# Optimization experiments

Hardware: AMD Instinct MI355X
Metric: run time of the kernel (lower is better)

The kernel has to match this reference:

```python
import jax, jax.numpy as jnp
import numpy as np
from jax import lax

DG, KH, KW = 8, 3, 3
STRIDE, PAD, DIL = 1, 1, 1


def setup_inputs() -> dict:
    key = jax.random.key(0)
    ks = jax.random.split(key, 6)
    B, C, H, W = 4, 256, 64, 64
    Cout = 256
    off_ch = DG * 3 * KH * KW  # 216
    x = jax.random.normal(ks[0], (B, C, H, W), dtype=jnp.float32)
    extra_feat = jax.random.normal(ks[1], (B, C, H, W), dtype=jnp.float32)
    weight = jax.random.normal(ks[2], (Cout, C, KH, KW), dtype=jnp.float32) * 0.02
    bias = jax.random.normal(ks[3], (Cout,), dtype=jnp.float32) * 0.01
    off_w = jax.random.normal(ks[4], (off_ch, C, KH, KW), dtype=jnp.float32) * 0.01
    off_b = jax.random.normal(ks[5], (off_ch,), dtype=jnp.float32) * 0.01
    return {"x": x, "extra_feat": extra_feat, "weight": weight, "bias": bias,
            "off_w": off_w, "off_b": off_b}


def _modulated_deform_conv(x, offset, mask, weight, bias):
    B, C, H, W = x.shape
    Cout = weight.shape[0]
    K = KH * KW
    Ho, Wo = offset.shape[2], offset.shape[3]
    Cg = C // DG

    # offset: [B, 2*DG*K, Ho, Wo] interpreted as (dg, K, (dy, dx)) interleaved
    off = offset.reshape(B, DG, K, 2, Ho, Wo)
    dy, dx = off[:, :, :, 0], off[:, :, :, 1]  # [B, DG, K, Ho, Wo]

    ky = jnp.repeat(jnp.arange(KH), KW)  # [K]
    kx = jnp.tile(jnp.arange(KW), KH)    # [K]
    base_y = (jnp.arange(Ho) * STRIDE - PAD)[None, None, None, :, None] + (ky * DIL)[None, None, :, None, None]
    base_x = (jnp.arange(Wo) * STRIDE - PAD)[None, None, None, None, :] + (kx * DIL)[None, None, :, None, None]
    py = dy + base_y  # [B, DG, K, Ho, Wo]
    px = dx + base_x

    y0f = jnp.floor(py)
    x0f = jnp.floor(px)
    fy = py - y0f
    fx = px - x0f
    y0 = y0f.astype(jnp.int32)
    x0 = x0f.astype(jnp.int32)

    xg = x.reshape(B, DG, Cg, H * W)
    N = K * Ho * Wo

    def gather(yi, xi):
        valid = ((yi >= 0) & (yi < H) & (xi >= 0) & (xi < W)).astype(x.dtype)
        idx = (jnp.clip(yi, 0, H - 1) * W + jnp.clip(xi, 0, W - 1)).reshape(B, DG, 1, N)
        g = jnp.take_along_axis(xg, jnp.broadcast_to(idx, (B, DG, Cg, N)), axis=-1)
        g = g.reshape(B, DG, Cg, K, Ho, Wo)
        return g * valid[:, :, None]

    val = (((1 - fy) * (1 - fx))[:, :, None] * gather(y0, x0)
           + ((1 - fy) * fx)[:, :, None] * gather(y0, x0 + 1)
           + (fy * (1 - fx))[:, :, None] * gather(y0 + 1, x0)
           + (fy * fx)[:, :, None] * gather(y0 + 1, x0 + 1))
    val = val * mask.reshape(B, DG, 1, K, Ho, Wo)
    val = val.reshape(B, C, K, Ho, Wo)

    out = jnp.einsum('bckhw,ock->bohw', val, weight.reshape(Cout, C, K))
    return out + bias[None, :, None, None]


def reference(x, extra_feat, weight, bias, off_w, off_b):
    # conv_offset: plain conv predicting offsets + mask
    om = lax.conv_general_dilated(
        extra_feat, off_w, window_strides=(STRIDE, STRIDE),
        padding=((PAD, PAD), (PAD, PAD)), rhs_dilation=(DIL, DIL),
        dimension_numbers=('NCHW', 'OIHW', 'NCHW')) + off_b[None, :, None, None]
    o1, o2, mask = jnp.split(om, 3, axis=1)
    offset = jnp.concatenate([o1, o2], axis=1)
    mask = jax.nn.sigmoid(mask)
    return _modulated_deform_conv(x, offset, mask, weight, bias)
```

## Files before the change

### kernel.cpp

```cpp
#include <hip/hip_runtime.h>
#include <hip/hip_bf16.h>
#include <math.h>

#define BB 4
#define CC 256
#define HH 64
#define WW 64
#define HW 4096
#define PH 68
#define PW 68
#define COUT 256
#define OFFC 216
#define KTOT 2304
#define NCHUNK 72

typedef __attribute__((ext_vector_type(4))) float f32x4;
typedef __attribute__((ext_vector_type(8))) short s16x8;
typedef __attribute__((ext_vector_type(8))) unsigned short u16x8;
typedef __attribute__((ext_vector_type(2))) unsigned int u32x2;

__device__ __forceinline__ unsigned short f2bf(float f) {
    unsigned int u = __float_as_uint(f);
    return (unsigned short)((u + 0x7fffu + ((u >> 16) & 1u)) >> 16);
}
__device__ __forceinline__ float bflo(unsigned int u) { return __uint_as_float(u << 16); }
__device__ __forceinline__ float bfhi(unsigned int u) { return __uint_as_float(u & 0xffff0000u); }
__device__ __forceinline__ unsigned int pkbf(float a, float b) {
    __hip_bfloat162 h = __float22bfloat162_rn(make_float2(a, b));
    unsigned int r;
    __builtin_memcpy(&r, &h, 4);
    return r;
}

#define WAITL() asm volatile("s_waitcnt lgkmcnt(0)" ::: "memory")
#define RBAR() __builtin_amdgcn_s_barrier()

__global__ __launch_bounds__(256) void pack_w_main(const float* __restrict__ w,
                                                   unsigned short* __restrict__ wp) {
    int idx = blockIdx.x * 256 + threadIdx.x;
    int t = idx >> 13, r = idx & 8191;
    int oc = r >> 5, s = (r >> 3) & 3, e = r & 7;
    int kk = ((s ^ ((oc >> 1) & 3)) << 3) | e;
    int dg = t / 9, tap = t - dg * 9;
    int c = dg * 32 + kk;
    wp[idx] = f2bf(w[((size_t)oc * CC + c) * 9 + tap]);
}

__global__ __launch_bounds__(256) void pack_w_off(const float* __restrict__ w,
                                                  unsigned short* __restrict__ wp) {
    int idx = blockIdx.x * 256 + threadIdx.x;
    int t = idx >> 13, r = idx & 8191;
    int oc = r >> 5, s = (r >> 3) & 3, e = r & 7;
    int kk = ((s ^ ((oc >> 1) & 3)) << 3) | e;
    int tap = t >> 3, cg = t & 7;
    int c = cg * 32 + kk;
    float v = (oc < OFFC) ? w[((size_t)oc * CC + c) * 9 + tap] : 0.f;
    wp[idx] = f2bf(v);
}

__global__ __launch_bounds__(256) void pad_tr2(const float* __restrict__ srcx,
                                               const float* __restrict__ srce,
                                               unsigned short* __restrict__ dx_,
                                               unsigned short* __restrict__ de_) {
    const float* src = blockIdx.y ? srce : srcx;
    unsigned short* dst = blockIdx.y ? de_ : dx_;
    int blk = blockIdx.x;
    int b = blk / PH, yp = blk % PH;
    int y = yp - 2;
    unsigned short* drow = dst + ((size_t)b * PH + yp) * PW * CC;
    int tid = threadIdx.x;
    if ((unsigned)y >= (unsigned)HH) {
        for (int i = tid; i < PW * CC / 8; i += 256) *(u16x8*)&drow[(size_t)i * 8] = (u16x8)0;
        return;
    }
    __shared__ float tile[64][65];
    int lane = tid & 63, w = tid >> 6;
    int oct = tid & 7, xi = tid >> 3;
    const float* srow = src + (size_t)b * CC * HW + (size_t)y * WW;
    for (int chunk = 0; chunk < 4; chunk++) {
        __syncthreads();
#pragma unroll
        for (int i = 0; i < 16; i++) {
            int c = chunk * 64 + w * 16 + i;
            tile[w * 16 + i][lane] = srow[(size_t)c * HW + lane];
        }
        __syncthreads();
#pragma unroll
        for (int xq = 0; xq < 3; xq++) {
            int xp = xq * 32 + xi;
            if (xp < PW) {
                int x = xp - 2;
                u16x8 v = (u16x8)0;
                if ((unsigned)x < (unsigned)WW) {
#pragma unroll
                    for (int e = 0; e < 8; e++) v[e] = f2bf(tile[oct * 8 + e][x]);
                }
                *(u16x8*)&drow[(size_t)xp * CC + chunk * 64 + oct * 8] = v;
            }
        }
    }
}


#define A_LOAD(WPP, T, AF)                                                \
    {                                                                     \
        const unsigned short* wt_ = WPP + (size_t)(T) * 8192 + aoff;      \
        AF[0] = *(const s16x8*)&wt_[0];                                   \
        AF[1] = *(const s16x8*)&wt_[512];                                 \
        AF[2] = *(const s16x8*)&wt_[8192];                                \
        AF[3] = *(const s16x8*)&wt_[8704];                                \
    }

#define MFMA8R(AC, BUF)                                                                      \
    {                                                                                        \
        int sw_ = (lg ^ ((r16 >> 1) & 3)) << 3;                                              \
        s16x8 b0_ = *(const s16x8*)&sB[BUF][0][r16 * 32 + sw_];                              \
        s16x8 b1_ = *(const s16x8*)&sB[BUF][0][(16 + r16) * 32 + sw_];                       \
        acc[0][0] = __builtin_amdgcn_mfma_f32_16x16x32_bf16(AC[0], b0_, acc[0][0], 0, 0, 0); \
        acc[0][1] = __builtin_amdgcn_mfma_f32_16x16x32_bf16(AC[0], b1_, acc[0][1], 0, 0, 0); \
        acc[1][0] = __builtin_amdgcn_mfma_f32_16x16x32_bf16(AC[1], b0_, acc[1][0], 0, 0, 0); \
        acc[1][1] = __builtin_amdgcn_mfma_f32_16x16x32_bf16(AC[1], b1_, acc[1][1], 0, 0, 0); \
        b0_ = *(const s16x8*)&sB[BUF][1][r16 * 32 + sw_];                                    \
        b1_ = *(const s16x8*)&sB[BUF][1][(16 + r16) * 32 + sw_];                             \
        acc[0][0] = __builtin_amdgcn_mfma_f32_16x16x32_bf16(AC[2], b0_, acc[0][0], 0, 0, 0); \
        acc[0][1] = __builtin_amdgcn_mfma_f32_16x16x32_bf16(AC[2], b1_, acc[0][1], 0, 0, 0); \
        acc[1][0] = __builtin_amdgcn_mfma_f32_16x16x32_bf16(AC[3], b0_, acc[1][0], 0, 0, 0); \
        acc[1][1] = __builtin_amdgcn_mfma_f32_16x16x32_bf16(AC[3], b1_, acc[1][1], 0, 0, 0); \
    }

__global__ __launch_bounds__(512, 4) void fused_dcn(const unsigned short* __restrict__ eT,
                                                    const unsigned short* __restrict__ xT,
                                                    const unsigned short* __restrict__ wpo,
                                                    const unsigned short* __restrict__ wpm,
                                                    const float* __restrict__ off_b,
                                                    const float* __restrict__ bias,
                                                    float* __restrict__ out) {
    __shared__ __align__(16) unsigned short sB[2][2][1024];
    __shared__ unsigned int sOP[NCHUNK][32][3];

    int bx = blockIdx.x;
    int b = bx >> 6, y = bx & 63;
    int pxh = blockIdx.y;
    int tid = threadIdx.x;
    int lane = tid & 63;
    int w = tid >> 6;
    int r16 = lane & 15, lg = lane >> 4;
    int aoff = (w * 32 + r16) * 32 + ((lg ^ ((r16 >> 1) & 3)) << 3);
    int p1px = tid >> 4, ch2 = tid & 15;
    int pxg = pxh * 32 + p1px;
    int kt = tid >> 8;
    int p2px = (tid >> 3) & 31;
    int ch4 = tid & 7;

    const unsigned short* eb = eT + (size_t)b * PH * PW * CC;
    const unsigned short* xb = xT + (size_t)b * PH * PW * CC;

    f32x4 acc[2][2];
#pragma unroll
    for (int mi = 0; mi < 2; mi++)
#pragma unroll
        for (int ni = 0; ni < 2; ni++) acc[mi][ni] = (f32x4)0.f;

    s16x8 aA[4], aB[4];

#define BSLOT2 (p1px * 32 + ((((ch2 >> 2) ^ ((p1px >> 1) & 3))) << 3) + (ch2 & 3) * 2)
#define OF_B(T, BV)                                                                          \
    {                                                                                        \
        int tap_ = (T) >> 3, cg_ = (T) & 7;                                                  \
        int ky_ = tap_ / 3, kx_ = tap_ - ky_ * 3;                                            \
        BV = *(const unsigned int*)&eb[(size_t)((y + ky_ + 1) * PW + (pxg + kx_ + 1)) * CC + \
                                       cg_ * 32 + ch2 * 2];                                  \
    }
#define OF_ITF(T, BUF, AC, AN, BP0, BP1, BN0, BN1)               \
    {                                                            \
        A_LOAD(wpo, (T) + 2, AN)                                 \
        OF_B((T) + 4, BN0)                                       \
        OF_B((T) + 5, BN1)                                       \
        MFMA8R(AC, BUF)                                          \
        *(unsigned int*)&sB[(BUF) ^ 1][0][BSLOT2] = BP0;         \
        *(unsigned int*)&sB[(BUF) ^ 1][1][BSLOT2] = BP1;         \
        WAITL();                                                 \
        RBAR();                                                  \
    }

    {
        unsigned int bP0, bP1, bN0, bN1;
        {
            A_LOAD(wpo, 0, aA)
            unsigned int c0, c1;
            OF_B(0, c0)
            OF_B(1, c1)
            *(unsigned int*)&sB[0][0][BSLOT2] = c0;
            *(unsigned int*)&sB[0][1][BSLOT2] = c1;
            OF_B(2, bP0)
            OF_B(3, bP1)
            WAITL();
            RBAR();
        }
        for (int t = 0; t < 68; t += 4) {
            OF_ITF(t, 0, aA, aB, bP0, bP1, bN0, bN1)
            OF_ITF(t + 2, 1, aB, aA, bN0, bN1, bP0, bP1)
        }
        {
            A_LOAD(wpo, 70, aB)
            MFMA8R(aA, 0)
            *(unsigned int*)&sB[1][0][BSLOT2] = bP0;
            *(unsigned int*)&sB[1][1][BSLOT2] = bP1;
            WAITL();
            RBAR();
        }
        MFMA8R(aB, 1)
    }

    __syncthreads();
#pragma unroll
    for (int mi = 0; mi < 2; mi++) {
#pragma unroll
        for (int ni = 0; ni < 2; ni++) {
#pragma unroll
            for (int j = 0; j < 4; j++) {
                int oc = w * 32 + mi * 16 + lg * 4 + j;
                if (oc < OFFC) {
                    int dg, tap, comp;
                    if (oc < 144) {
                        dg = oc / 18;
                        int rr = oc - dg * 18;
                        tap = rr >> 1;
                        comp = rr & 1;
                    } else {
                        int o2 = oc - 144;
                        dg = o2 / 9;
                        tap = o2 - dg * 9;
                        comp = 2;
                    }
                    sOP[dg * 9 + tap][ni * 16 + r16][comp] =
                        __float_as_uint(acc[mi][ni][j] + off_b[oc]);
                }
            }
        }
    }
    __syncthreads();
    for (int i = tid; i < NCHUNK * 32; i += 512) {
        int tt = i >> 5, px = i & 31;
        int dg = (tt * 57) >> 9;
        int tap = tt - dg * 9;
        int ky = tap / 3, kx = tap - ky * 3;
        float dyv = __uint_as_float(sOP[tt][px][0]);
        float dxv = __uint_as_float(sOP[tt][px][1]);
        float mr = __uint_as_float(sOP[tt][px][2]);
        int xg = pxh * 32 + px;
        float mv = 1.f / (1.f + __expf(-mr));
        float py = (float)(y + ky - 1) + dyv;
        float pxx = (float)(xg + kx - 1) + dxv;
        float y0f = floorf(py), x0f = floorf(pxx);
        float fy = py - y0f, fx = pxx - x0f;
        int yp0 = min(max((int)y0f + 2, 0), PH - 1);
        int yp1 = min(max((int)y0f + 3, 0), PH - 1);
        int xp0 = min(max((int)x0f + 2, 0), PW - 1);
        int xp1 = min(max((int)x0f + 3, 0), PW - 1);
        float w00 = (1.f - fy) * (1.f - fx) * mv;
        float w01 = (1.f - fy) * fx * mv;
        float w10 = fy * (1.f - fx) * mv;
        float w11 = fy * fx * mv;
        sOP[tt][px][0] = (unsigned int)(yp0 * PW + xp0) | ((unsigned int)(xp1 - xp0) << 13) |
                         ((unsigned int)(yp1 - yp0) << 14);
        sOP[tt][px][1] = pkbf(w00, w01);
        sOP[tt][px][2] = pkbf(w10, w11);
    }
    __syncthreads();

#pragma unroll
    for (int mi = 0; mi < 2; mi++)
#pragma unroll
        for (int ni = 0; ni < 2; ni++) acc[mi][ni] = (f32x4)0.f;

#define BSLOT4 (p2px * 32 + ((((ch4 >> 1) ^ ((p2px >> 1) & 3))) << 3) + (ch4 & 1) * 4)
#define DC_G(T, G00, G01, G10, G11)                                       \
    {                                                                     \
        int dg_ = ((T) * 57) >> 9;                                        \
        unsigned int iv_ = sOP[T][p2px][0];                               \
        int o00_ = (int)(iv_ & 8191u) << 8;                               \
        int dxe_ = (int)((iv_ >> 13) & 1u) << 8;                          \
        int dye_ = ((iv_ >> 14) & 1u) ? (PW * CC) : 0;                    \
        const unsigned short* p_ = xb + dg_ * 32 + ch4 * 4;               \
        G00 = *(const u32x2*)(p_ + o00_);                                 \
        G01 = *(const u32x2*)(p_ + o00_ + dxe_);                          \
        G10 = *(const u32x2*)(p_ + o00_ + dye_);                          \
        G11 = *(const u32x2*)(p_ + o00_ + dye_ + dxe_);                   \
    }
#define DC_FIN(T, G00, G01, G10, G11, BUF)                                                \
    {                                                                                     \
        unsigned int wa_ = sOP[T][p2px][1];                                               \
        unsigned int wb_ = sOP[T][p2px][2];                                               \
        float w00 = bflo(wa_), w01 = bfhi(wa_);                                           \
        float w10 = bflo(wb_), w11 = bfhi(wb_);                                           \
        float v0 = w00 * bflo(G00[0]) + w01 * bflo(G01[0]) + w10 * bflo(G10[0]) +         \
                   w11 * bflo(G11[0]);                                                    \
        float v1 = w00 * bfhi(G00[0]) + w01 * bfhi(G01[0]) + w10 * bfhi(G10[0]) +         \
                   w11 * bfhi(G11[0]);                                                    \
        float v2 = w00 * bflo(G00[1]) + w01 * bflo(G01[1]) + w10 * bflo(G10[1]) +         \
                   w11 * bflo(G11[1]);                                                    \
        float v3 = w00 * bfhi(G00[1]) + w01 * bfhi(G01[1]) + w10 * bfhi(G10[1]) +         \
                   w11 * bfhi(G11[1]);                                                    \
        u32x2 pk_;                                                                        \
        pk_[0] = pkbf(v0, v1);                                                            \
        pk_[1] = pkbf(v2, v3);                                                            \
        *(u32x2*)&sB[BUF][kt][BSLOT4] = pk_;                                              \
    }
#define DC_ITF(T, BUF, AC, AN, GP0, GP1, GP2, GP3, GN0, GN1, GN2, GN3)     \
    {                                                                      \
        A_LOAD(wpm, (T) + 2, AN)                                           \
        DC_G((T) + 4 + kt, GN0, GN1, GN2, GN3)                             \
        MFMA8R(AC, BUF)                                                    \
        DC_FIN((T) + 2 + kt, GP0, GP1, GP2, GP3, (BUF) ^ 1)                \
        WAITL();                                                           \
        RBAR();                                                            \
    }

    {
        u32x2 gA0, gA1, gA2, gA3, gB0, gB1, gB2, gB3;
        {
            A_LOAD(wpm, 0, aA)
            u32x2 t0, t1, t2, t3;
            DC_G(kt, t0, t1, t2, t3)
            DC_FIN(kt, t0, t1, t2, t3, 0)
            DC_G(2 + kt, gA0, gA1, gA2, gA3)
            WAITL();
            RBAR();
        }
        for (int t = 0; t < 64; t += 4) {
            DC_ITF(t, 0, aA, aB, gA0, gA1, gA2, gA3, gB0, gB1, gB2, gB3)
            DC_ITF(t + 2, 1, aB, aA, gB0, gB1, gB2, gB3, gA0, gA1, gA2, gA3)
        }
        DC_ITF(64, 0, aA, aB, gA0, gA1, gA2, gA3, gB0, gB1, gB2, gB3)
        DC_ITF(66, 1, aB, aA, gB0, gB1, gB2, gB3, gA0, gA1, gA2, gA3)
        {
            A_LOAD(wpm, 70, aB)
            MFMA8R(aA, 0)
            DC_FIN(70 + kt, gA0, gA1, gA2, gA3, 1)
            WAITL();
            RBAR();
        }
        MFMA8R(aB, 1)
    }

#pragma unroll
    for (int mi = 0; mi < 2; mi++) {
#pragma unroll
        for (int ni = 0; ni < 2; ni++) {
#pragma unroll
            for (int j = 0; j < 4; j++) {
                int oc = w * 32 + mi * 16 + lg * 4 + j;
                int pxo = pxh * 32 + ni * 16 + r16;
                out[(size_t)(b * COUT + oc) * HW + y * WW + pxo] = acc[mi][ni][j] + bias[oc];
            }
        }
    }
}

extern "C" void kernel_launch(void* const* d_in, const int* in_sizes, int n_in,
                              void* d_out, int out_size, void* d_ws, size_t ws_size,
                              hipStream_t stream) {
    const float* x = (const float*)d_in[0];
    const float* extra_feat = (const float*)d_in[1];
    const float* weight = (const float*)d_in[2];
    const float* bias = (const float*)d_in[3];
    const float* off_w = (const float*)d_in[4];
    const float* off_b = (const float*)d_in[5];
    float* out = (float*)d_out;

    unsigned short* wpm = (unsigned short*)d_ws;
    unsigned short* wpo = wpm + (size_t)KTOT * COUT;
    unsigned short* xT = wpo + (size_t)KTOT * COUT;
    unsigned short* eT = xT + (size_t)BB * PH * PW * CC;

    pack_w_main<<<(KTOT * COUT) / 256, 256, 0, stream>>>(weight, wpm);
    pack_w_off<<<(KTOT * COUT) / 256, 256, 0, stream>>>(off_w, wpo);
    pad_tr2<<<dim3(BB * PH, 2), 256, 0, stream>>>(x, extra_feat, xT, eT);

    fused_dcn<<<dim3(BB * HH, 2), 512, 0, stream>>>(eT, xT, wpo, wpm, off_b, bias, out);
}
```

Baseline: 90.36 us.

## Double threads per block and split pixel columns across waves

The fused kernel now launches 1024 threads (16 waves) instead of 512, and the work is split so each wave owns 32 output channels by 16 pixels rather than 32 by 32. Each thread also gathers half as much data per tap (2 channels instead of 4), so the bilinear sampling work is spread over twice as many threads. The goal is more latency hiding for the gathers and more waves to interleave the MFMAs with the sampling. In exchange, every A-fragment load from global memory is repeated by two waves, each wave issues fewer MFMAs between barriers, and barrier cost goes up with the larger block.

```diff
diff --git a/kernel.cpp b/kernel.cpp
--- a/kernel.cpp
+++ b/kernel.cpp
@@ -17,7 +17,6 @@
 typedef __attribute__((ext_vector_type(4))) float f32x4;
 typedef __attribute__((ext_vector_type(8))) short s16x8;
 typedef __attribute__((ext_vector_type(8))) unsigned short u16x8;
-typedef __attribute__((ext_vector_type(2))) unsigned int u32x2;
 
 __device__ __forceinline__ unsigned short f2bf(float f) {
     unsigned int u = __float_as_uint(f);
@@ -111,30 +110,24 @@
         AF[3] = *(const s16x8*)&wt_[8704];                                \
     }
 
-#define MFMA8R(AC, BUF)                                                                      \
+#define MFMA4R(AC, BUF)                                                                      \
     {                                                                                        \
         int sw_ = (lg ^ ((r16 >> 1) & 3)) << 3;                                              \
-        s16x8 b0_ = *(const s16x8*)&sB[BUF][0][r16 * 32 + sw_];                              \
-        s16x8 b1_ = *(const s16x8*)&sB[BUF][0][(16 + r16) * 32 + sw_];                       \
-        acc[0][0] = __builtin_amdgcn_mfma_f32_16x16x32_bf16(AC[0], b0_, acc[0][0], 0, 0, 0); \
-        acc[0][1] = __builtin_amdgcn_mfma_f32_16x16x32_bf16(AC[0], b1_, acc[0][1], 0, 0, 0); \
-        acc[1][0] = __builtin_amdgcn_mfma_f32_16x16x32_bf16(AC[1], b0_, acc[1][0], 0, 0, 0); \
-        acc[1][1] = __builtin_amdgcn_mfma_f32_16x16x32_bf16(AC[1], b1_, acc[1][1], 0, 0, 0); \
-        b0_ = *(const s16x8*)&sB[BUF][1][r16 * 32 + sw_];                                    \
-        b1_ = *(const s16x8*)&sB[BUF][1][(16 + r16) * 32 + sw_];                             \
-        acc[0][0] = __builtin_amdgcn_mfma_f32_16x16x32_bf16(AC[2], b0_, acc[0][0], 0, 0, 0); \
-        acc[0][1] = __builtin_amdgcn_mfma_f32_16x16x32_bf16(AC[2], b1_, acc[0][1], 0, 0, 0); \
-        acc[1][0] = __builtin_amdgcn_mfma_f32_16x16x32_bf16(AC[3], b0_, acc[1][0], 0, 0, 0); \
-        acc[1][1] = __builtin_amdgcn_mfma_f32_16x16x32_bf16(AC[3], b1_, acc[1][1], 0, 0, 0); \
-    }
-
-__global__ __launch_bounds__(512, 4) void fused_dcn(const unsigned short* __restrict__ eT,
-                                                    const unsigned short* __restrict__ xT,
-                                                    const unsigned short* __restrict__ wpo,
-                                                    const unsigned short* __restrict__ wpm,
-                                                    const float* __restrict__ off_b,
-                                                    const float* __restrict__ bias,
-                                                    float* __restrict__ out) {
+        s16x8 b0_ = *(const s16x8*)&sB[BUF][0][(wn * 16 + r16) * 32 + sw_];                  \
+        acc[0] = __builtin_amdgcn_mfma_f32_16x16x32_bf16(AC[0], b0_, acc[0], 0, 0, 0);       \
+        acc[1] = __builtin_amdgcn_mfma_f32_16x16x32_bf16(AC[1], b0_, acc[1], 0, 0, 0);       \
+        b0_ = *(const s16x8*)&sB[BUF][1][(wn * 16 + r16) * 32 + sw_];                        \
+        acc[0] = __builtin_amdgcn_mfma_f32_16x16x32_bf16(AC[2], b0_, acc[0], 0, 0, 0);       \
+        acc[1] = __builtin_amdgcn_mfma_f32_16x16x32_bf16(AC[3], b0_, acc[1], 0, 0, 0);       \
+    }
+
+__global__ __launch_bounds__(1024, 8) void fused_dcn(const unsigned short* __restrict__ eT,
+                                                     const unsigned short* __restrict__ xT,
+                                                     const unsigned short* __restrict__ wpo,
+                                                     const unsigned short* __restrict__ wpm,
+                                                     const float* __restrict__ off_b,
+                                                     const float* __restrict__ bias,
+                                                     float* __restrict__ out) {
     __shared__ __align__(16) unsigned short sB[2][2][1024];
     __shared__ unsigned int sOP[NCHUNK][32][3];
 
@@ -144,26 +137,25 @@
     int tid = threadIdx.x;
     int lane = tid & 63;
     int w = tid >> 6;
+    int wm = w & 7, wn = w >> 3;
     int r16 = lane & 15, lg = lane >> 4;
-    int aoff = (w * 32 + r16) * 32 + ((lg ^ ((r16 >> 1) & 3)) << 3);
-    int p1px = tid >> 4, ch2 = tid & 15;
-    int pxg = pxh * 32 + p1px;
-    int kt = tid >> 8;
-    int p2px = (tid >> 3) & 31;
-    int ch4 = tid & 7;
+    int aoff = (wm * 32 + r16) * 32 + ((lg ^ ((r16 >> 1) & 3)) << 3);
+    int ktc = tid >> 9;
+    int spx = (tid >> 4) & 31;
+    int ch2 = tid & 15;
+    int pxg = pxh * 32 + spx;
 
     const unsigned short* eb = eT + (size_t)b * PH * PW * CC;
     const unsigned short* xb = xT + (size_t)b * PH * PW * CC;
 
-    f32x4 acc[2][2];
-#pragma unroll
-    for (int mi = 0; mi < 2; mi++)
-#pragma unroll
-        for (int ni = 0; ni < 2; ni++) acc[mi][ni] = (f32x4)0.f;
+    f32x4 acc[2];
+    acc[0] = (f32x4)0.f;
+    acc[1] = (f32x4)0.f;
 
     s16x8 aA[4], aB[4];
 
-#define BSLOT2 (p1px * 32 + ((((ch2 >> 2) ^ ((p1px >> 1) & 3))) << 3) + (ch2 & 3) * 2)
+#define BSLOT (spx * 32 + (((ch2 >> 2) ^ ((spx >> 1) & 3)) << 3) + (ch2 & 3) * 2)
+
 #define OF_B(T, BV)                                                                          \
     {                                                                                        \
         int tap_ = (T) >> 3, cg_ = (T) & 7;                                                  \
@@ -171,76 +163,67 @@
         BV = *(const unsigned int*)&eb[(size_t)((y + ky_ + 1) * PW + (pxg + kx_ + 1)) * CC + \
                                        cg_ * 32 + ch2 * 2];                                  \
     }
-#define OF_ITF(T, BUF, AC, AN, BP0, BP1, BN0, BN1)               \
+#define OF_ITF(T, BUF, AC, AN, BP, BN)                           \
     {                                                            \
         A_LOAD(wpo, (T) + 2, AN)                                 \
-        OF_B((T) + 4, BN0)                                       \
-        OF_B((T) + 5, BN1)                                       \
-        MFMA8R(AC, BUF)                                          \
-        *(unsigned int*)&sB[(BUF) ^ 1][0][BSLOT2] = BP0;         \
-        *(unsigned int*)&sB[(BUF) ^ 1][1][BSLOT2] = BP1;         \
+        OF_B((T) + 4 + ktc, BN)                                  \
+        MFMA4R(AC, BUF)                                          \
+        *(unsigned int*)&sB[(BUF) ^ 1][ktc][BSLOT] = BP;         \
         WAITL();                                                 \
         RBAR();                                                  \
     }
 
     {
-        unsigned int bP0, bP1, bN0, bN1;
+        unsigned int bP, bN;
         {
             A_LOAD(wpo, 0, aA)
-            unsigned int c0, c1;
-            OF_B(0, c0)
-            OF_B(1, c1)
-            *(unsigned int*)&sB[0][0][BSLOT2] = c0;
-            *(unsigned int*)&sB[0][1][BSLOT2] = c1;
-            OF_B(2, bP0)
-            OF_B(3, bP1)
+            unsigned int c0;
+            OF_B(ktc, c0)
+            *(unsigned int*)&sB[0][ktc][BSLOT] = c0;
+            OF_B(2 + ktc, bP)
             WAITL();
             RBAR();
         }
         for (int t = 0; t < 68; t += 4) {
-            OF_ITF(t, 0, aA, aB, bP0, bP1, bN0, bN1)
-            OF_ITF(t + 2, 1, aB, aA, bN0, bN1, bP0, bP1)
+            OF_ITF(t, 0, aA, aB, bP, bN)
+            OF_ITF(t + 2, 1, aB, aA, bN, bP)
         }
         {
             A_LOAD(wpo, 70, aB)
-            MFMA8R(aA, 0)
-            *(unsigned int*)&sB[1][0][BSLOT2] = bP0;
-            *(unsigned int*)&sB[1][1][BSLOT2] = bP1;
+            MFMA4R(aA, 0)
+            *(unsigned int*)&sB[1][ktc][BSLOT] = bP;
             WAITL();
             RBAR();
         }
-        MFMA8R(aB, 1)
+        MFMA4R(aB, 1)
     }
 
     __syncthreads();
 #pragma unroll
     for (int mi = 0; mi < 2; mi++) {
 #pragma unroll
-        for (int ni = 0; ni < 2; ni++) {
-#pragma unroll
-            for (int j = 0; j < 4; j++) {
-                int oc = w * 32 + mi * 16 + lg * 4 + j;
-                if (oc < OFFC) {
-                    int dg, tap, comp;
-                    if (oc < 144) {
-                        dg = oc / 18;
-                        int rr = oc - dg * 18;
-                        tap = rr >> 1;
-                        comp = rr & 1;
-                    } else {
-                        int o2 = oc - 144;
-                        dg = o2 / 9;
-                        tap = o2 - dg * 9;
-                        comp = 2;
-                    }
-                    sOP[dg * 9 + tap][ni * 16 + r16][comp] =
-                        __float_as_uint(acc[mi][ni][j] + off_b[oc]);
+        for (int j = 0; j < 4; j++) {
+            int oc = wm * 32 + mi * 16 + lg * 4 + j;
+            if (oc < OFFC) {
+                int dg, tap, comp;
+                if (oc < 144) {
+                    dg = oc / 18;
+                    int rr = oc - dg * 18;
+                    tap = rr >> 1;
+                    comp = rr & 1;
+                } else {
+                    int o2 = oc - 144;
+                    dg = o2 / 9;
+                    tap = o2 - dg * 9;
+                    comp = 2;
                 }
+                sOP[dg * 9 + tap][wn * 16 + r16][comp] =
+                    __float_as_uint(acc[mi][j] + off_b[oc]);
             }
         }
     }
     __syncthreads();
-    for (int i = tid; i < NCHUNK * 32; i += 512) {
+    for (int i = tid; i < NCHUNK * 32; i += 1024) {
         int tt = i >> 5, px = i & 31;
         int dg = (tt * 57) >> 9;
         int tap = tt - dg * 9;
@@ -269,62 +252,50 @@
     }
     __syncthreads();
 
-#pragma unroll
-    for (int mi = 0; mi < 2; mi++)
-#pragma unroll
-        for (int ni = 0; ni < 2; ni++) acc[mi][ni] = (f32x4)0.f;
-
-#define BSLOT4 (p2px * 32 + ((((ch4 >> 1) ^ ((p2px >> 1) & 3))) << 3) + (ch4 & 1) * 4)
+    acc[0] = (f32x4)0.f;
+    acc[1] = (f32x4)0.f;
+
 #define DC_G(T, G00, G01, G10, G11)                                       \
     {                                                                     \
         int dg_ = ((T) * 57) >> 9;                                        \
-        unsigned int iv_ = sOP[T][p2px][0];                               \
+        unsigned int iv_ = sOP[T][spx][0];                                \
         int o00_ = (int)(iv_ & 8191u) << 8;                               \
         int dxe_ = (int)((iv_ >> 13) & 1u) << 8;                          \
         int dye_ = ((iv_ >> 14) & 1u) ? (PW * CC) : 0;                    \
-        const unsigned short* p_ = xb + dg_ * 32 + ch4 * 4;               \
-        G00 = *(const u32x2*)(p_ + o00_);                                 \
-        G01 = *(const u32x2*)(p_ + o00_ + dxe_);                          \
-        G10 = *(const u32x2*)(p_ + o00_ + dye_);                          \
-        G11 = *(const u32x2*)(p_ + o00_ + dye_ + dxe_);                   \
+        const unsigned short* p_ = xb + dg_ * 32 + ch2 * 2;               \
+        G00 = *(const unsigned int*)(p_ + o00_);                          \
+        G01 = *(const unsigned int*)(p_ + o00_ + dxe_);                   \
+        G10 = *(const unsigned int*)(p_ + o00_ + dye_);                   \
+        G11 = *(const unsigned int*)(p_ + o00_ + dye_ + dxe_);            \
     }
 #define DC_FIN(T, G00, G01, G10, G11, BUF)                                                \
     {                                                                                     \
-        unsigned int wa_ = sOP[T][p2px][1];                                               \
-        unsigned int wb_ = sOP[T][p2px][2];                                               \
+        unsigned int wa_ = sOP[T][spx][1];                                                \
+        unsigned int wb_ = sOP[T][spx][2];                                                \
         float w00 = bflo(wa_), w01 = bfhi(wa_);                                           \
         float w10 = bflo(wb_), w11 = bfhi(wb_);                                           \
-        float v0 = w00 * bflo(G00[0]) + w01 * bflo(G01[0]) + w10 * bflo(G10[0]) +         \
-                   w11 * bflo(G11[0]);                                                    \
-        float v1 = w00 * bfhi(G00[0]) + w01 * bfhi(G01[0]) + w10 * bfhi(G10[0]) +         \
-                   w11 * bfhi(G11[0]);                                                    \
-        float v2 = w00 * bflo(G00[1]) + w01 * bflo(G01[1]) + w10 * bflo(G10[1]) +         \
-                   w11 * bflo(G11[1]);                                                    \
-        float v3 = w00 * bfhi(G00[1]) + w01 * bfhi(G01[1]) + w10 * bfhi(G10[1]) +         \
-                   w11 * bfhi(G11[1]);                                                    \
-        u32x2 pk_;                                                                        \
-        pk_[0] = pkbf(v0, v1);                                                            \
-        pk_[1] = pkbf(v2, v3);                                                            \
-        *(u32x2*)&sB[BUF][kt][BSLOT4] = pk_;                                              \
+        float v0 = w00 * bflo(G00) + w01 * bflo(G01) + w10 * bflo(G10) + w11 * bflo(G11); \
+        float v1 = w00 * bfhi(G00) + w01 * bfhi(G01) + w10 * bfhi(G10) + w11 * bfhi(G11); \
+        *(unsigned int*)&sB[BUF][ktc][BSLOT] = pkbf(v0, v1);                              \
     }
 #define DC_ITF(T, BUF, AC, AN, GP0, GP1, GP2, GP3, GN0, GN1, GN2, GN3)     \
     {                                                                      \
         A_LOAD(wpm, (T) + 2, AN)                                           \
-        DC_G((T) + 4 + kt, GN0, GN1, GN2, GN3)                             \
-        MFMA8R(AC, BUF)                                                    \
-        DC_FIN((T) + 2 + kt, GP0, GP1, GP2, GP3, (BUF) ^ 1)                \
+        DC_G((T) + 4 + ktc, GN0, GN1, GN2, GN3)                            \
+        MFMA4R(AC, BUF)                                                    \
+        DC_FIN((T) + 2 + ktc, GP0, GP1, GP2, GP3, (BUF) ^ 1)               \
         WAITL();                                                           \
         RBAR();                                                            \
     }
 
     {
-        u32x2 gA0, gA1, gA2, gA3, gB0, gB1, gB2, gB3;
+        unsigned int gA0, gA1, gA2, gA3, gB0, gB1, gB2, gB3;
         {
             A_LOAD(wpm, 0, aA)
-            u32x2 t0, t1, t2, t3;
-            DC_G(kt, t0, t1, t2, t3)
-            DC_FIN(kt, t0, t1, t2, t3, 0)
-            DC_G(2 + kt, gA0, gA1, gA2, gA3)
+            unsigned int t0, t1, t2, t3;
+            DC_G(ktc, t0, t1, t2, t3)
+            DC_FIN(ktc, t0, t1, t2, t3, 0)
+            DC_G(2 + ktc, gA0, gA1, gA2, gA3)
             WAITL();
             RBAR();
         }
@@ -336,24 +307,21 @@
         DC_ITF(66, 1, aB, aA, gB0, gB1, gB2, gB3, gA0, gA1, gA2, gA3)
         {
             A_LOAD(wpm, 70, aB)
-            MFMA8R(aA, 0)
-            DC_FIN(70 + kt, gA0, gA1, gA2, gA3, 1)
+            MFMA4R(aA, 0)
+            DC_FIN(70 + ktc, gA0, gA1, gA2, gA3, 1)
             WAITL();
             RBAR();
         }
-        MFMA8R(aB, 1)
+        MFMA4R(aB, 1)
     }
 
 #pragma unroll
     for (int mi = 0; mi < 2; mi++) {
 #pragma unroll
-        for (int ni = 0; ni < 2; ni++) {
-#pragma unroll
-            for (int j = 0; j < 4; j++) {
-                int oc = w * 32 + mi * 16 + lg * 4 + j;
-                int pxo = pxh * 32 + ni * 16 + r16;
-                out[(size_t)(b * COUT + oc) * HW + y * WW + pxo] = acc[mi][ni][j] + bias[oc];
-            }
+        for (int j = 0; j < 4; j++) {
+            int oc = wm * 32 + mi * 16 + lg * 4 + j;
+            int pxo = pxh * 32 + wn * 16 + r16;
+            out[(size_t)(b * COUT + oc) * HW + y * WW + pxo] = acc[mi][j] + bias[oc];
         }
     }
 }
@@ -378,5 +346,5 @@
     pack_w_off<<<(KTOT * COUT) / 256, 256, 0, stream>>>(off_w, wpo);
     pad_tr2<<<dim3(BB * PH, 2), 256, 0, stream>>>(x, extra_feat, xT, eT);
 
-    fused_dcn<<<dim3(BB * HH, 2), 512, 0, stream>>>(eT, xT, wpo, wpm, off_b, bias, out);
-}
+    fused_dcn<<<dim3(BB * HH, 2), 1024, 0, stream>>>(eT, xT, wpo, wpm, off_b, bias, out);
+}
```

New measurement: 127.5 us. 1.41x slower.

## Widen fused DCN block tile to a full 64-pixel output row

Applied to the files above, without the earlier changes.

Each block now covers a whole 64-pixel output row instead of half a row, so the grid shrinks to 256 blocks and each wave holds 2x4 MFMA accumulators. The weight A-fragments are loaded once per row rather than twice, which halves the weight traffic from global memory. Gather and interpolation work is remapped so each thread handles both K-halves for one pixel, and shared-memory buffers are doubled. The trade-off is fewer blocks (256 on a 256-CU part, one block per CU) and higher register and LDS use, with launch bounds lowered to 2 blocks per CU.

```diff
diff --git a/kernel.cpp b/kernel.cpp
--- a/kernel.cpp
+++ b/kernel.cpp
@@ -18,6 +18,10 @@
 typedef __attribute__((ext_vector_type(8))) short s16x8;
 typedef __attribute__((ext_vector_type(8))) unsigned short u16x8;
 typedef __attribute__((ext_vector_type(2))) unsigned int u32x2;
+
+struct G4 {
+    u32x2 c00, c01, c10, c11;
+};
 
 __device__ __forceinline__ unsigned short f2bf(float f) {
     unsigned int u = __float_as_uint(f);
@@ -111,87 +115,110 @@
         AF[3] = *(const s16x8*)&wt_[8704];                                \
     }
 
-#define MFMA8R(AC, BUF)                                                                      \
-    {                                                                                        \
-        int sw_ = (lg ^ ((r16 >> 1) & 3)) << 3;                                              \
-        s16x8 b0_ = *(const s16x8*)&sB[BUF][0][r16 * 32 + sw_];                              \
-        s16x8 b1_ = *(const s16x8*)&sB[BUF][0][(16 + r16) * 32 + sw_];                       \
-        acc[0][0] = __builtin_amdgcn_mfma_f32_16x16x32_bf16(AC[0], b0_, acc[0][0], 0, 0, 0); \
-        acc[0][1] = __builtin_amdgcn_mfma_f32_16x16x32_bf16(AC[0], b1_, acc[0][1], 0, 0, 0); \
-        acc[1][0] = __builtin_amdgcn_mfma_f32_16x16x32_bf16(AC[1], b0_, acc[1][0], 0, 0, 0); \
-        acc[1][1] = __builtin_amdgcn_mfma_f32_16x16x32_bf16(AC[1], b1_, acc[1][1], 0, 0, 0); \
-        b0_ = *(const s16x8*)&sB[BUF][1][r16 * 32 + sw_];                                    \
-        b1_ = *(const s16x8*)&sB[BUF][1][(16 + r16) * 32 + sw_];                             \
-        acc[0][0] = __builtin_amdgcn_mfma_f32_16x16x32_bf16(AC[2], b0_, acc[0][0], 0, 0, 0); \
-        acc[0][1] = __builtin_amdgcn_mfma_f32_16x16x32_bf16(AC[2], b1_, acc[0][1], 0, 0, 0); \
-        acc[1][0] = __builtin_amdgcn_mfma_f32_16x16x32_bf16(AC[3], b0_, acc[1][0], 0, 0, 0); \
-        acc[1][1] = __builtin_amdgcn_mfma_f32_16x16x32_bf16(AC[3], b1_, acc[1][1], 0, 0, 0); \
-    }
-
-__global__ __launch_bounds__(512, 4) void fused_dcn(const unsigned short* __restrict__ eT,
+#define MFMA16R(AC, BUF)                                                                      \
+    {                                                                                         \
+        int sw_ = (lg ^ ((r16 >> 1) & 3)) << 3;                                               \
+        _Pragma("unroll") for (int kti = 0; kti < 2; kti++) {                                 \
+            _Pragma("unroll") for (int ni = 0; ni < 4; ni++) {                                \
+                s16x8 b_ = *(const s16x8*)&sB[BUF][kti][(ni * 16 + r16) * 32 + sw_];          \
+                acc[0][ni] = __builtin_amdgcn_mfma_f32_16x16x32_bf16(AC[kti * 2], b_,         \
+                                                                     acc[0][ni], 0, 0, 0);    \
+                acc[1][ni] = __builtin_amdgcn_mfma_f32_16x16x32_bf16(AC[kti * 2 + 1], b_,     \
+                                                                     acc[1][ni], 0, 0, 0);    \
+            }                                                                                 \
+        }                                                                                     \
+    }
+
+#define BSLOT (spx * 32 + (((ch4 >> 1) ^ ((spx >> 1) & 3)) << 3) + (ch4 & 1) * 4)
+
+__device__ __forceinline__ void dc_g(const unsigned short* p, const unsigned int* sop, G4& g) {
+    unsigned int iv = sop[0];
+    int o00 = (int)(iv & 8191u) << 8;
+    int dxe = (int)((iv >> 13) & 1u) << 8;
+    int dye = ((iv >> 14) & 1u) ? (PW * CC) : 0;
+    g.c00 = *(const u32x2*)(p + o00);
+    g.c01 = *(const u32x2*)(p + o00 + dxe);
+    g.c10 = *(const u32x2*)(p + o00 + dye);
+    g.c11 = *(const u32x2*)(p + o00 + dye + dxe);
+}
+__device__ __forceinline__ void dc_fin(const unsigned int* sop, const G4& g,
+                                       unsigned short* dst) {
+    unsigned int wa = sop[1], wb = sop[2];
+    float w00 = bflo(wa), w01 = bfhi(wa);
+    float w10 = bflo(wb), w11 = bfhi(wb);
+    float v0 = w00 * bflo(g.c00[0]) + w01 * bflo(g.c01[0]) + w10 * bflo(g.c10[0]) +
+               w11 * bflo(g.c11[0]);
+    float v1 = w00 * bfhi(g.c00[0]) + w01 * bfhi(g.c01[0]) + w10 * bfhi(g.c10[0]) +
+               w11 * bfhi(g.c11[0]);
+    float v2 = w00 * bflo(g.c00[1]) + w01 * bflo(g.c01[1]) + w10 * bflo(g.c10[1]) +
+               w11 * bflo(g.c11[1]);
+    float v3 = w00 * bfhi(g.c00[1]) + w01 * bfhi(g.c01[1]) + w10 * bfhi(g.c10[1]) +
+               w11 * bfhi(g.c11[1]);
+    u32x2 pk;
+    pk[0] = pkbf(v0, v1);
+    pk[1] = pkbf(v2, v3);
+    *(u32x2*)dst = pk;
+}
+
+__global__ __launch_bounds__(512, 2) void fused_dcn(const unsigned short* __restrict__ eT,
                                                     const unsigned short* __restrict__ xT,
                                                     const unsigned short* __restrict__ wpo,
                                                     const unsigned short* __restrict__ wpm,
                                                     const float* __restrict__ off_b,
                                                     const float* __restrict__ bias,
                                                     float* __restrict__ out) {
-    __shared__ __align__(16) unsigned short sB[2][2][1024];
-    __shared__ unsigned int sOP[NCHUNK][32][3];
+    __shared__ __align__(16) unsigned short sB[2][2][2048];
+    __shared__ unsigned int sOP[NCHUNK][64][3];
 
     int bx = blockIdx.x;
     int b = bx >> 6, y = bx & 63;
-    int pxh = blockIdx.y;
     int tid = threadIdx.x;
     int lane = tid & 63;
-    int w = tid >> 6;
+    int wm = tid >> 6;
     int r16 = lane & 15, lg = lane >> 4;
-    int aoff = (w * 32 + r16) * 32 + ((lg ^ ((r16 >> 1) & 3)) << 3);
-    int p1px = tid >> 4, ch2 = tid & 15;
-    int pxg = pxh * 32 + p1px;
-    int kt = tid >> 8;
-    int p2px = (tid >> 3) & 31;
+    int aoff = (wm * 32 + r16) * 32 + ((lg ^ ((r16 >> 1) & 3)) << 3);
+    int spx = tid >> 3;
     int ch4 = tid & 7;
 
     const unsigned short* eb = eT + (size_t)b * PH * PW * CC;
     const unsigned short* xb = xT + (size_t)b * PH * PW * CC;
 
-    f32x4 acc[2][2];
+    f32x4 acc[2][4];
 #pragma unroll
     for (int mi = 0; mi < 2; mi++)
 #pragma unroll
-        for (int ni = 0; ni < 2; ni++) acc[mi][ni] = (f32x4)0.f;
+        for (int ni = 0; ni < 4; ni++) acc[mi][ni] = (f32x4)0.f;
 
     s16x8 aA[4], aB[4];
 
-#define BSLOT2 (p1px * 32 + ((((ch2 >> 2) ^ ((p1px >> 1) & 3))) << 3) + (ch2 & 3) * 2)
-#define OF_B(T, BV)                                                                          \
-    {                                                                                        \
-        int tap_ = (T) >> 3, cg_ = (T) & 7;                                                  \
-        int ky_ = tap_ / 3, kx_ = tap_ - ky_ * 3;                                            \
-        BV = *(const unsigned int*)&eb[(size_t)((y + ky_ + 1) * PW + (pxg + kx_ + 1)) * CC + \
-                                       cg_ * 32 + ch2 * 2];                                  \
+#define OF_B(T, BV)                                                                         \
+    {                                                                                       \
+        int tap_ = (T) >> 3, cg_ = (T) & 7;                                                 \
+        int ky_ = tap_ / 3, kx_ = tap_ - ky_ * 3;                                           \
+        BV = *(const u32x2*)&eb[(size_t)((y + ky_ + 1) * PW + (spx + kx_ + 1)) * CC +       \
+                                cg_ * 32 + ch4 * 4];                                        \
     }
 #define OF_ITF(T, BUF, AC, AN, BP0, BP1, BN0, BN1)               \
     {                                                            \
         A_LOAD(wpo, (T) + 2, AN)                                 \
         OF_B((T) + 4, BN0)                                       \
         OF_B((T) + 5, BN1)                                       \
-        MFMA8R(AC, BUF)                                          \
-        *(unsigned int*)&sB[(BUF) ^ 1][0][BSLOT2] = BP0;         \
-        *(unsigned int*)&sB[(BUF) ^ 1][1][BSLOT2] = BP1;         \
+        MFMA16R(AC, BUF)                                         \
+        *(u32x2*)&sB[(BUF) ^ 1][0][BSLOT] = BP0;                 \
+        *(u32x2*)&sB[(BUF) ^ 1][1][BSLOT] = BP1;                 \
         WAITL();                                                 \
         RBAR();                                                  \
     }
 
     {
-        unsigned int bP0, bP1, bN0, bN1;
+        u32x2 bP0, bP1, bN0, bN1;
         {
             A_LOAD(wpo, 0, aA)
-            unsigned int c0, c1;
+            u32x2 c0, c1;
             OF_B(0, c0)
             OF_B(1, c1)
-            *(unsigned int*)&sB[0][0][BSLOT2] = c0;
-            *(unsigned int*)&sB[0][1][BSLOT2] = c1;
+            *(u32x2*)&sB[0][0][BSLOT] = c0;
+            *(u32x2*)&sB[0][1][BSLOT] = c1;
             OF_B(2, bP0)
             OF_B(3, bP1)
             WAITL();
@@ -203,23 +230,23 @@
         }
         {
             A_LOAD(wpo, 70, aB)
-            MFMA8R(aA, 0)
-            *(unsigned int*)&sB[1][0][BSLOT2] = bP0;
-            *(unsigned int*)&sB[1][1][BSLOT2] = bP1;
+            MFMA16R(aA, 0)
+            *(u32x2*)&sB[1][0][BSLOT] = bP0;
+            *(u32x2*)&sB[1][1][BSLOT] = bP1;
             WAITL();
             RBAR();
         }
-        MFMA8R(aB, 1)
+        MFMA16R(aB, 1)
     }
 
     __syncthreads();
 #pragma unroll
     for (int mi = 0; mi < 2; mi++) {
 #pragma unroll
-        for (int ni = 0; ni < 2; ni++) {
+        for (int ni = 0; ni < 4; ni++) {
 #pragma unroll
             for (int j = 0; j < 4; j++) {
-                int oc = w * 32 + mi * 16 + lg * 4 + j;
+                int oc = wm * 32 + mi * 16 + lg * 4 + j;
                 if (oc < OFFC) {
                     int dg, tap, comp;
                     if (oc < 144) {
@@ -240,18 +267,17 @@
         }
     }
     __syncthreads();
-    for (int i = tid; i < NCHUNK * 32; i += 512) {
-        int tt = i >> 5, px = i & 31;
+    for (int i = tid; i < NCHUNK * 64; i += 512) {
+        int tt = i >> 6, px = i & 63;
         int dg = (tt * 57) >> 9;
         int tap = tt - dg * 9;
         int ky = tap / 3, kx = tap - ky * 3;
         float dyv = __uint_as_float(sOP[tt][px][0]);
         float dxv = __uint_as_float(sOP[tt][px][1]);
         float mr = __uint_as_float(sOP[tt][px][2]);
-        int xg = pxh * 32 + px;
         float mv = 1.f / (1.f + __expf(-mr));
         float py = (float)(y + ky - 1) + dyv;
-        float pxx = (float)(xg + kx - 1) + dxv;
+        float pxx = (float)(px + kx - 1) + dxv;
         float y0f = floorf(py), x0f = floorf(pxx);
         float fy = py - y0f, fx = pxx - x0f;
         int yp0 = min(max((int)y0f + 2, 0), PH - 1);
@@ -272,86 +298,61 @@
 #pragma unroll
     for (int mi = 0; mi < 2; mi++)
 #pragma unroll
-        for (int ni = 0; ni < 2; ni++) acc[mi][ni] = (f32x4)0.f;
-
-#define BSLOT4 (p2px * 32 + ((((ch4 >> 1) ^ ((p2px >> 1) & 3))) << 3) + (ch4 & 1) * 4)
-#define DC_G(T, G00, G01, G10, G11)                                       \
-    {                                                                     \
-        int dg_ = ((T) * 57) >> 9;                                        \
-        unsigned int iv_ = sOP[T][p2px][0];                               \
-        int o00_ = (int)(iv_ & 8191u) << 8;                               \
-        int dxe_ = (int)((iv_ >> 13) & 1u) << 8;                          \
-        int dye_ = ((iv_ >> 14) & 1u) ? (PW * CC) : 0;                    \
-        const unsigned short* p_ = xb + dg_ * 32 + ch4 * 4;               \
-        G00 = *(const u32x2*)(p_ + o00_);                                 \
-        G01 = *(const u32x2*)(p_ + o00_ + dxe_);                          \
-        G10 = *(const u32x2*)(p_ + o00_ + dye_);                          \
-        G11 = *(const u32x2*)(p_ + o00_ + dye_ + dxe_);                   \
-    }
-#define DC_FIN(T, G00, G01, G10, G11, BUF)                                                \
-    {                                                                                     \
-        unsigned int wa_ = sOP[T][p2px][1];                                               \
-        unsigned int wb_ = sOP[T][p2px][2];                                               \
-        float w00 = bflo(wa_), w01 = bfhi(wa_);                                           \
-        float w10 = bflo(wb_), w11 = bfhi(wb_);                                           \
-        float v0 = w00 * bflo(G00[0]) + w01 * bflo(G01[0]) + w10 * bflo(G10[0]) +         \
-                   w11 * bflo(G11[0]);                                                    \
-        float v1 = w00 * bfhi(G00[0]) + w01 * bfhi(G01[0]) + w10 * bfhi(G10[0]) +         \
-                   w11 * bfhi(G11[0]);                                                    \
-        float v2 = w00 * bflo(G00[1]) + w01 * bflo(G01[1]) + w10 * bflo(G10[1]) +         \
-                   w11 * bflo(G11[1]);                                                    \
-        float v3 = w00 * bfhi(G00[1]) + w01 * bfhi(G01[1]) + w10 * bfhi(G10[1]) +         \
-                   w11 * bfhi(G11[1]);                                                    \
-        u32x2 pk_;                                                                        \
-        pk_[0] = pkbf(v0, v1);                                                            \
-        pk_[1] = pkbf(v2, v3);                                                            \
-        *(u32x2*)&sB[BUF][kt][BSLOT4] = pk_;                                              \
-    }
-#define DC_ITF(T, BUF, AC, AN, GP0, GP1, GP2, GP3, GN0, GN1, GN2, GN3)     \
-    {                                                                      \
-        A_LOAD(wpm, (T) + 2, AN)                                           \
-        DC_G((T) + 4 + kt, GN0, GN1, GN2, GN3)                             \
-        MFMA8R(AC, BUF)                                                    \
-        DC_FIN((T) + 2 + kt, GP0, GP1, GP2, GP3, (BUF) ^ 1)                \
-        WAITL();                                                           \
-        RBAR();                                                            \
+        for (int ni = 0; ni < 4; ni++) acc[mi][ni] = (f32x4)0.f;
+
+#define XP(T) (xb + (((T) * 57) >> 9) * 32 + ch4 * 4)
+
+#define DC_ITF(T, BUF, AC, AN, GP0, GP1, GN0, GN1)                   \
+    {                                                                \
+        A_LOAD(wpm, (T) + 2, AN)                                     \
+        dc_g(XP((T) + 4), &sOP[(T) + 4][spx][0], GN0);               \
+        dc_g(XP((T) + 5), &sOP[(T) + 5][spx][0], GN1);               \
+        MFMA16R(AC, BUF)                                             \
+        dc_fin(&sOP[(T) + 2][spx][0], GP0, &sB[(BUF) ^ 1][0][BSLOT]);\
+        dc_fin(&sOP[(T) + 3][spx][0], GP1, &sB[(BUF) ^ 1][1][BSLOT]);\
+        WAITL();                                                     \
+        RBAR();                                                      \
     }
 
     {
-        u32x2 gA0, gA1, gA2, gA3, gB0, gB1, gB2, gB3;
+        G4 gA0, gA1, gB0, gB1;
         {
             A_LOAD(wpm, 0, aA)
-            u32x2 t0, t1, t2, t3;
-            DC_G(kt, t0, t1, t2, t3)
-            DC_FIN(kt, t0, t1, t2, t3, 0)
-            DC_G(2 + kt, gA0, gA1, gA2, gA3)
+            G4 t0, t1;
+            dc_g(XP(0), &sOP[0][spx][0], t0);
+            dc_g(XP(1), &sOP[1][spx][0], t1);
+            dc_fin(&sOP[0][spx][0], t0, &sB[0][0][BSLOT]);
+            dc_fin(&sOP[1][spx][0], t1, &sB[0][1][BSLOT]);
+            dc_g(XP(2), &sOP[2][spx][0], gA0);
+            dc_g(XP(3), &sOP[3][spx][0], gA1);
             WAITL();
             RBAR();
         }
         for (int t = 0; t < 64; t += 4) {
-            DC_ITF(t, 0, aA, aB, gA0, gA1, gA2, gA3, gB0, gB1, gB2, gB3)
-            DC_ITF(t + 2, 1, aB, aA, gB0, gB1, gB2, gB3, gA0, gA1, gA2, gA3)
-        }
-        DC_ITF(64, 0, aA, aB, gA0, gA1, gA2, gA3, gB0, gB1, gB2, gB3)
-        DC_ITF(66, 1, aB, aA, gB0, gB1, gB2, gB3, gA0, gA1, gA2, gA3)
+            DC_ITF(t, 0, aA, aB, gA0, gA1, gB0, gB1)
+            DC_ITF(t + 2, 1, aB, aA, gB0, gB1, gA0, gA1)
+        }
+        DC_ITF(64, 0, aA, aB, gA0, gA1, gB0, gB1)
+        DC_ITF(66, 1, aB, aA, gB0, gB1, gA0, gA1)
         {
             A_LOAD(wpm, 70, aB)
-            MFMA8R(aA, 0)
-            DC_FIN(70 + kt, gA0, gA1, gA2, gA3, 1)
+            MFMA16R(aA, 0)
+            dc_fin(&sOP[70][spx][0], gA0, &sB[1][0][BSLOT]);
+            dc_fin(&sOP[71][spx][0], gA1, &sB[1][1][BSLOT]);
             WAITL();
             RBAR();
         }
-        MFMA8R(aB, 1)
+        MFMA16R(aB, 1)
     }
 
 #pragma unroll
     for (int mi = 0; mi < 2; mi++) {
 #pragma unroll
-        for (int ni = 0; ni < 2; ni++) {
+        for (int ni = 0; ni < 4; ni++) {
 #pragma unroll
             for (int j = 0; j < 4; j++) {
-                int oc = w * 32 + mi * 16 + lg * 4 + j;
-                int pxo = pxh * 32 + ni * 16 + r16;
+                int oc = wm * 32 + mi * 16 + lg * 4 + j;
+                int pxo = ni * 16 + r16;
                 out[(size_t)(b * COUT + oc) * HW + y * WW + pxo] = acc[mi][ni][j] + bias[oc];
             }
         }
@@ -378,5 +379,5 @@
     pack_w_off<<<(KTOT * COUT) / 256, 256, 0, stream>>>(off_w, wpo);
     pad_tr2<<<dim3(BB * PH, 2), 256, 0, stream>>>(x, extra_feat, xT, eT);
 
-    fused_dcn<<<dim3(BB * HH, 2), 512, 0, stream>>>(eT, xT, wpo, wpm, off_b, bias, out);
-}
+    fused_dcn<<<BB * HH, 512, 0, stream>>>(eT, xT, wpo, wpm, off_b, bias, out);
+}
```

Result: slower. 92.19 us (+2.0%).

## Load offset-conv B fragments directly from global into registers, dropping LDS staging

Applied to the files above, without the earlier changes.

The offset-convolution GEMM phase no longer stages the extra_feat B tiles through double-buffered shared memory with barriers. Each lane now loads its 16-byte MFMA B fragment straight from global memory and issues the MFMAs right away. This removes the LDS writes, LDS reads and the per-chunk block barriers. In exchange, the software pipelining that overlapped the next chunk's loads with the current MFMAs is gone, so global load latency may be exposed and each wave loads B redundantly.

```diff
diff --git a/kernel.cpp b/kernel.cpp
--- a/kernel.cpp
+++ b/kernel.cpp
@@ -146,8 +146,6 @@
     int w = tid >> 6;
     int r16 = lane & 15, lg = lane >> 4;
     int aoff = (w * 32 + r16) * 32 + ((lg ^ ((r16 >> 1) & 3)) << 3);
-    int p1px = tid >> 4, ch2 = tid & 15;
-    int pxg = pxh * 32 + p1px;
     int kt = tid >> 8;
     int p2px = (tid >> 3) & 31;
     int ch4 = tid & 7;
@@ -163,53 +161,33 @@
 
     s16x8 aA[4], aB[4];
 
-#define BSLOT2 (p1px * 32 + ((((ch2 >> 2) ^ ((p1px >> 1) & 3))) << 3) + (ch2 & 3) * 2)
-#define OF_B(T, BV)                                                                          \
-    {                                                                                        \
-        int tap_ = (T) >> 3, cg_ = (T) & 7;                                                  \
-        int ky_ = tap_ / 3, kx_ = tap_ - ky_ * 3;                                            \
-        BV = *(const unsigned int*)&eb[(size_t)((y + ky_ + 1) * PW + (pxg + kx_ + 1)) * CC + \
-                                       cg_ * 32 + ch2 * 2];                                  \
-    }
-#define OF_ITF(T, BUF, AC, AN, BP0, BP1, BN0, BN1)               \
-    {                                                            \
-        A_LOAD(wpo, (T) + 2, AN)                                 \
-        OF_B((T) + 4, BN0)                                       \
-        OF_B((T) + 5, BN1)                                       \
-        MFMA8R(AC, BUF)                                          \
-        *(unsigned int*)&sB[(BUF) ^ 1][0][BSLOT2] = BP0;         \
-        *(unsigned int*)&sB[(BUF) ^ 1][1][BSLOT2] = BP1;         \
-        WAITL();                                                 \
-        RBAR();                                                  \
-    }
-
-    {
-        unsigned int bP0, bP1, bN0, bN1;
-        {
-            A_LOAD(wpo, 0, aA)
-            unsigned int c0, c1;
-            OF_B(0, c0)
-            OF_B(1, c1)
-            *(unsigned int*)&sB[0][0][BSLOT2] = c0;
-            *(unsigned int*)&sB[0][1][BSLOT2] = c1;
-            OF_B(2, bP0)
-            OF_B(3, bP1)
-            WAITL();
-            RBAR();
-        }
-        for (int t = 0; t < 68; t += 4) {
-            OF_ITF(t, 0, aA, aB, bP0, bP1, bN0, bN1)
-            OF_ITF(t + 2, 1, aB, aA, bN0, bN1, bP0, bP1)
-        }
-        {
-            A_LOAD(wpo, 70, aB)
-            MFMA8R(aA, 0)
-            *(unsigned int*)&sB[1][0][BSLOT2] = bP0;
-            *(unsigned int*)&sB[1][1][BSLOT2] = bP1;
-            WAITL();
-            RBAR();
-        }
-        MFMA8R(aB, 1)
+    for (int t = 0; t < NCHUNK; t += 2) {
+        A_LOAD(wpo, t, aA)
+        s16x8 bf[4];
+#pragma unroll
+        for (int kti = 0; kti < 2; kti++) {
+            int tt = t + kti;
+            int tap_ = tt >> 3, cg_ = tt & 7;
+            int ky_ = tap_ / 3, kx_ = tap_ - ky_ * 3;
+#pragma unroll
+            for (int ni = 0; ni < 2; ni++) {
+                int px_ = pxh * 32 + ni * 16 + r16;
+                bf[kti * 2 + ni] = *(const s16x8*)&eb[(size_t)((y + ky_ + 1) * PW +
+                                                               (px_ + kx_ + 1)) * CC +
+                                                      cg_ * 32 + lg * 8];
+            }
+        }
+#pragma unroll
+        for (int kti = 0; kti < 2; kti++) {
+#pragma unroll
+            for (int ni = 0; ni < 2; ni++) {
+                acc[0][ni] = __builtin_amdgcn_mfma_f32_16x16x32_bf16(aA[kti * 2], bf[kti * 2 + ni],
+                                                                     acc[0][ni], 0, 0, 0);
+                acc[1][ni] = __builtin_amdgcn_mfma_f32_16x16x32_bf16(aA[kti * 2 + 1],
+                                                                     bf[kti * 2 + ni],
+                                                                     acc[1][ni], 0, 0, 0);
+            }
+        }
     }
 
     __syncthreads();
```

Result: slower. 144.8 us (+60.3%).
